# Performance work log

Measured on AMD Instinct MI355X. Metric: run time of the kernel, lower is better.

The kernel has to match this reference:

```python
import jax, jax.numpy as jnp
import numpy as np

N_QUBITS = 12
N_LAYERS = 5
OUTPUT_DIM = 4
BATCH = 1024


def _apply_1q(state, U, q, n):
    # state: (B, 2^n) complex; U: (B, 2, 2) per-sample unitary on wire q
    B = state.shape[0]
    s = state.reshape(B, 2 ** q, 2, -1)
    s = jnp.einsum('bik,bakc->baic', U, s)
    return s.reshape(B, -1)


def _cnot(state, c, t, n):
    # CNOT with control wire c, target wire t (wire 0 = most significant bit)
    B = state.shape[0]
    s = state.reshape((B,) + (2,) * n)
    s0 = jax.lax.index_in_dim(s, 0, axis=1 + c, keepdims=True)
    s1 = jax.lax.index_in_dim(s, 1, axis=1 + c, keepdims=True)
    s1 = jnp.flip(s1, axis=1 + t)  # X on target where control = 1
    return jnp.concatenate([s0, s1], axis=1 + c).reshape(B, -1)


def _forward(x, input_weights, theta, output_weights):
    n, L, D = N_QUBITS, N_LAYERS, OUTPUT_DIM
    x = jnp.tanh(x)
    B = x.shape[0]
    # |0...0> initial state, batched
    state = jnp.zeros((B, 2 ** n), jnp.complex64).at[:, 0].set(1.0)
    for l in range(L):
        # data re-uploading: RX(input_weights[l,j] * x[:,j]) on every wire, every layer
        a = input_weights[l][None, :] * x          # (B, n) RX angles
        b = theta[l, :, 0]                          # (n,) RY angles
        c = theta[l, :, 1]                          # (n,) RZ angles
        ca = jnp.cos(a / 2).astype(jnp.complex64)
        sa = jnp.sin(a / 2).astype(jnp.complex64)
        Rx = jnp.stack([jnp.stack([ca, -1j * sa], -1),
                        jnp.stack([-1j * sa, ca], -1)], -2)  # (B, n, 2, 2)
        cb = jnp.cos(b / 2).astype(jnp.complex64)
        sb = jnp.sin(b / 2).astype(jnp.complex64)
        ec = jnp.exp(-1j * c.astype(jnp.complex64) / 2)      # e^{-i c/2}
        # M = RZ(c) @ RY(b), shared across the batch
        M = jnp.stack([jnp.stack([ec * cb, -ec * sb], -1),
                       jnp.stack([jnp.conj(ec) * sb, jnp.conj(ec) * cb], -1)], -2)  # (n,2,2)
        # fused single-qubit unitary U = RZ @ RY @ RX per (sample, wire)
        U = jnp.einsum('qik,bqkj->bqij', M, Rx)
        for q in range(n):
            state = _apply_1q(state, U[:, q], q, n)
        for i in range(n):
            state = _cnot(state, i, (i + 1) % n, n)
    # exact <Z_i> on the first D wires
    p = jnp.abs(state) ** 2  # (B, 2^n)
    zs = []
    for i in range(D):
        pr = p.reshape(B, 2 ** i, 2, -1)
        zs.append(pr[:, :, 0, :].sum((1, 2)) - pr[:, :, 1, :].sum((1, 2)))
    Q = jnp.stack(zs, axis=1)  # (B, D)
    return output_weights[None, :] * Q


def setup_inputs() -> dict:
    key = jax.random.key(0)
    k1, k2, k3, k4 = jax.random.split(key, 4)
    return {
        'x': jax.random.normal(k1, (BATCH, N_QUBITS), jnp.float32),
        'input_weights': jax.random.normal(k2, (N_LAYERS, N_QUBITS), jnp.float32),
        'theta': jax.random.normal(k3, (N_LAYERS, N_QUBITS, 2), jnp.float32),
        'output_weights': jax.random.normal(k4, (OUTPUT_DIM,), jnp.float32),
    }


def reference(x, input_weights, theta, output_weights):
    return _forward(x, input_weights, theta, output_weights)
```

## Files before the change

kernel.cpp:

```cpp
#include <hip/hip_runtime.h>

#define NQ 12
#define NL 5
#define TPB 256


__device__ __forceinline__ void gate_pair(float2 &a, float2 &c,
        const float2 u00, const float2 u01, const float2 u10, const float2 u11) {
    float2 n0, n1;
    n0.x = fmaf(u00.x, a.x, fmaf(-u00.y, a.y, fmaf(u01.x, c.x, -u01.y * c.y)));
    n0.y = fmaf(u00.x, a.y, fmaf( u00.y, a.x, fmaf(u01.x, c.y,  u01.y * c.x)));
    n1.x = fmaf(u10.x, a.x, fmaf(-u10.y, a.y, fmaf(u11.x, c.x, -u11.y * c.y)));
    n1.y = fmaf(u10.x, a.y, fmaf( u10.y, a.x, fmaf(u11.x, c.y,  u11.y * c.x)));
    a = n0; c = n1;
}

template <int K>
__device__ __forceinline__ void apply_gate(float2 (&v)[16], const float2* __restrict__ Uq) {
    const float2 u00 = Uq[0], u01 = Uq[1], u10 = Uq[2], u11 = Uq[3];
#pragma unroll
    for (int h = 0; h < 8; ++h) {
        const int m0 = ((h >> K) << (K + 1)) | (h & ((1 << K) - 1));
        gate_pair(v[m0], v[m0 | (1 << K)], u00, u01, u10, u11);
    }
}

extern "C" __global__ void __launch_bounds__(TPB)
qnet_kernel(const float* __restrict__ x, const float* __restrict__ iw,
            const float* __restrict__ th, const float* __restrict__ ow,
            float* __restrict__ out) {
    __shared__ float2 st[4096];
    __shared__ float2 U[NL][NQ][4];
    __shared__ float wz[4][4];
    char* stb = (char*)st;

    const int b = blockIdx.x;
    const int tid = threadIdx.x;

    if (tid < NL * NQ) {
        const int l = tid / NQ, q = tid % NQ;
        const float xv = tanhf(x[b * NQ + q]);
        const float a = iw[l * NQ + q] * xv;
        const float bt = th[(l * NQ + q) * 2 + 0];
        const float ct = th[(l * NQ + q) * 2 + 1];
        float sa, ca; sincosf(0.5f * a, &sa, &ca);
        float sb, cb; sincosf(0.5f * bt, &sb, &cb);
        float sc, cc; sincosf(0.5f * ct, &sc, &cc);
        const float M00r = cc * cb, M00i = -sc * cb;
        const float M01r = -cc * sb, M01i = sc * sb;
        const float M10r = cc * sb, M10i = sc * sb;
        const float M11r = cc * cb, M11i = sc * cb;
        U[l][q][0] = make_float2(fmaf(M00r, ca,  sa * M01i), fmaf(M00i, ca, -sa * M01r));
        U[l][q][1] = make_float2(fmaf(ca, M01r,  sa * M00i), fmaf(ca, M01i, -sa * M00r));
        U[l][q][2] = make_float2(fmaf(M10r, ca,  sa * M11i), fmaf(M10i, ca, -sa * M11r));
        U[l][q][3] = make_float2(fmaf(ca, M11r,  sa * M10i), fmaf(ca, M11i, -sa * M10r));
    }

    const int baseA = (tid << 7) | ((tid & 7) << 4);
    const int baseB = ((tid >> 4) << 11) | ((tid & 15) << 3);
    const int baseC = (((tid >> 1) ^ ((tid >> 4) & 7)) << 4) | ((tid & 1) << 3);
    int pu = tid; pu ^= pu >> 1; pu ^= pu >> 2; pu ^= pu >> 4;
    const int Dt = pu ^ ((pu & 1) << 11);
    constexpr int CM[16] = {0x000,0x9FF,0xBFF,0x200,0xFFF,0x600,0x400,0xDFF,
                            0x7FF,0xE00,0xC00,0x5FF,0x800,0x1FF,0x3FF,0xA00};

    __syncthreads();

    float2 v[16];
    for (int l = 0; l < NL; ++l) {
        if (l == 0) {
#pragma unroll
            for (int r = 0; r < 16; ++r) v[r] = make_float2(0.f, 0.f);
            if (tid == 0) v[0].x = 1.f;
        } else {
#pragma unroll
            for (int c = 0; c < 8; ++c) {
                const float4 f = *(const float4*)(stb + (baseA ^ (c << 4)));
                v[2 * c]     = make_float2(f.x, f.y);
                v[2 * c + 1] = make_float2(f.z, f.w);
            }
        }
        apply_gate<0>(v, U[l][11]);
        apply_gate<1>(v, U[l][10]);
        apply_gate<2>(v, U[l][9]);
        apply_gate<3>(v, U[l][8]);
#pragma unroll
        for (int c = 0; c < 8; ++c) {
            *(float4*)(stb + (baseA ^ (c << 4))) =
                make_float4(v[2 * c].x, v[2 * c].y, v[2 * c + 1].x, v[2 * c + 1].y);
        }
        __syncthreads();

#pragma unroll
        for (int m = 0; m < 16; ++m)
            v[m] = *(const float2*)(stb + (baseB ^ ((m << 7) | ((m & 7) << 4))));
        apply_gate<0>(v, U[l][7]);
        apply_gate<1>(v, U[l][6]);
        apply_gate<2>(v, U[l][5]);
        apply_gate<3>(v, U[l][4]);
#pragma unroll
        for (int m = 0; m < 16; ++m)
            *(float2*)(stb + (baseB ^ ((m << 7) | ((m & 7) << 4)))) = v[m];
        __syncthreads();

#pragma unroll
        for (int m = 0; m < 16; ++m)
            v[m] = *(const float2*)(stb + baseC + (m << 11));
        apply_gate<0>(v, U[l][3]);
        apply_gate<1>(v, U[l][2]);
        apply_gate<2>(v, U[l][1]);
        apply_gate<3>(v, U[l][0]);
        __syncthreads();
#pragma unroll
        for (int m = 0; m < 16; ++m) {
            const int loc = Dt ^ CM[m];
            const int gl = loc >> 1;
            const int a = ((gl ^ ((gl >> 3) & 7)) << 4) | ((loc & 1) << 3);
            *(float2*)(stb + a) = v[m];
        }
        __syncthreads();
    }

    float ps = 0.f;
#pragma unroll
    for (int c = 0; c < 8; ++c) {
        const float4 f = *(const float4*)(stb + (baseA ^ (c << 4)));
        ps = fmaf(f.x, f.x, fmaf(f.y, f.y, fmaf(f.z, f.z, fmaf(f.w, f.w, ps))));
    }
    float s0 = (tid & 128) ? -ps : ps;
    float s1 = (tid & 64) ? -ps : ps;
    float s2 = (tid & 32) ? -ps : ps;
    float s3 = (tid & 16) ? -ps : ps;
#pragma unroll
    for (int off = 32; off > 0; off >>= 1) {
        s0 += __shfl_xor(s0, off);
        s1 += __shfl_xor(s1, off);
        s2 += __shfl_xor(s2, off);
        s3 += __shfl_xor(s3, off);
    }
    const int wave = tid >> 6;
    if ((tid & 63) == 0) {
        wz[wave][0] = s0; wz[wave][1] = s1; wz[wave][2] = s2; wz[wave][3] = s3;
    }
    __syncthreads();
    if (tid < 4) {
        const float z = wz[0][tid] + wz[1][tid] + wz[2][tid] + wz[3][tid];
        out[b * 4 + tid] = ow[tid] * z;
    }
}

extern "C" void kernel_launch(void* const* d_in, const int* in_sizes, int n_in,
                              void* d_out, int out_size, void* d_ws, size_t ws_size,
                              hipStream_t stream) {
    const float* x  = (const float*)d_in[0];
    const float* iw = (const float*)d_in[1];
    const float* th = (const float*)d_in[2];
    const float* ow = (const float*)d_in[3];
    float* out = (float*)d_out;
    const int batch = in_sizes[0] / NQ;
    hipLaunchKernelGGL(qnet_kernel, dim3(batch), dim3(TPB), 0, stream,
                       x, iw, th, ow, out);
}
```

Baseline: 47.35 us.

## Apply middle-qubit gates via DPP lane exchange to drop one LDS round-trip

Gates on wires 7,6 and 5,4 are now applied across lanes with DPP quad permutes, so each thread's amplitude set crosses lanes instead of going through shared memory. This removes one of the three shared-memory transpose phases and one barrier per layer. The swizzle and scatter addressing is rebuilt to match the new mapping. In exchange, each DPP gate does full-complex work on all 16 registers (twice the FMAs of a pair gate) and adds permute instructions.

```diff
diff --git a/kernel.cpp b/kernel.cpp
--- a/kernel.cpp
+++ b/kernel.cpp
@@ -4,6 +4,26 @@
 #define NL 5
 #define TPB 256
 
+__host__ __device__ constexpr int sfx12(int x) {
+    x ^= x >> 1; x ^= x >> 2; x ^= x >> 4; x ^= x >> 8;
+    return x & 0xFFF;
+}
+__host__ __device__ constexpr int amp_addr(int i) {
+    const int g = i >> 1;
+    const int G = g ^ ((g >> 3) & 7) ^ ((g >> 6) & 7);
+    return (G << 4) | ((i & 1) << 3);
+}
+__host__ __device__ constexpr int scat_c(int m) {
+    const int s = sfx12(m << 8);
+    return amp_addr(s ^ ((s & 1) << 11));
+}
+__host__ __device__ constexpr int p2_c(int m) { return amp_addr(m << 8); }
+
+template <int CTRL>
+__device__ __forceinline__ float dppx(float v) {
+    return __int_as_float(__builtin_amdgcn_update_dpp(
+        0, __float_as_int(v), CTRL, 0xF, 0xF, true));
+}
 
 __device__ __forceinline__ void gate_pair(float2 &a, float2 &c,
         const float2 u00, const float2 u01, const float2 u10, const float2 u11) {
@@ -25,17 +45,36 @@
     }
 }
 
+template <int CTRL, int LBIT>
+__device__ __forceinline__ void dpp_gate(float2 (&v)[16], const float2* __restrict__ Uq,
+                                         const int lane) {
+    const bool hi = (lane >> LBIT) & 1;
+    const float2 u00 = Uq[0], u01 = Uq[1], u10 = Uq[2], u11 = Uq[3];
+    const float2 co = hi ? u11 : u00;
+    const float2 cp = hi ? u10 : u01;
+#pragma unroll
+    for (int r = 0; r < 16; ++r) {
+        const float ox = v[r].x, oy = v[r].y;
+        const float px = dppx<CTRL>(ox);
+        const float py = dppx<CTRL>(oy);
+        v[r].x = fmaf(co.x, ox, fmaf(-co.y, oy, fmaf(cp.x, px, -cp.y * py)));
+        v[r].y = fmaf(co.x, oy, fmaf( co.y, ox, fmaf(cp.x, py,  cp.y * px)));
+    }
+}
+
 extern "C" __global__ void __launch_bounds__(TPB)
 qnet_kernel(const float* __restrict__ x, const float* __restrict__ iw,
             const float* __restrict__ th, const float* __restrict__ ow,
             float* __restrict__ out) {
     __shared__ float2 st[4096];
-    __shared__ float2 U[NL][NQ][4];
+    __shared__ __align__(16) float2 U[NL][NQ][4];
     __shared__ float wz[4][4];
     char* stb = (char*)st;
 
     const int b = blockIdx.x;
     const int tid = threadIdx.x;
+    const int Ln = tid & 63;
+    const int w  = tid >> 6;
 
     if (tid < NL * NQ) {
         const int l = tid / NQ, q = tid % NQ;
@@ -56,13 +95,11 @@
         U[l][q][3] = make_float2(fmaf(ca, M11r,  sa * M10i), fmaf(ca, M11i, -sa * M10r));
     }
 
-    const int baseA = (tid << 7) | ((tid & 7) << 4);
-    const int baseB = ((tid >> 4) << 11) | ((tid & 15) << 3);
-    const int baseC = (((tid >> 1) ^ ((tid >> 4) & 7)) << 4) | ((tid & 1) << 3);
-    int pu = tid; pu ^= pu >> 1; pu ^= pu >> 2; pu ^= pu >> 4;
-    const int Dt = pu ^ ((pu & 1) << 11);
-    constexpr int CM[16] = {0x000,0x9FF,0xBFF,0x200,0xFFF,0x600,0x400,0xDFF,
-                            0x7FF,0xE00,0xC00,0x5FF,0x800,0x1FF,0x3FF,0xA00};
+    const int base1 = amp_addr(tid << 4);
+    const int T2 = ((Ln & 3) << 6) | (w << 4) | (Ln >> 2);
+    const int base2 = amp_addr(T2);
+    const int sT = sfx12(T2);
+    const int baseS = amp_addr(sT ^ ((sT & 1) << 11));
 
     __syncthreads();
 
@@ -75,7 +112,7 @@
         } else {
 #pragma unroll
             for (int c = 0; c < 8; ++c) {
-                const float4 f = *(const float4*)(stb + (baseA ^ (c << 4)));
+                const float4 f = *(const float4*)(stb + (base1 ^ (c << 4)));
                 v[2 * c]     = make_float2(f.x, f.y);
                 v[2 * c + 1] = make_float2(f.z, f.w);
             }
@@ -84,47 +121,34 @@
         apply_gate<1>(v, U[l][10]);
         apply_gate<2>(v, U[l][9]);
         apply_gate<3>(v, U[l][8]);
+        dpp_gate<0xB1, 0>(v, U[l][7], Ln);
+        dpp_gate<0x4E, 1>(v, U[l][6], Ln);
 #pragma unroll
-        for (int c = 0; c < 8; ++c) {
-            *(float4*)(stb + (baseA ^ (c << 4))) =
+        for (int c = 0; c < 8; ++c)
+            *(float4*)(stb + (base1 ^ (c << 4))) =
                 make_float4(v[2 * c].x, v[2 * c].y, v[2 * c + 1].x, v[2 * c + 1].y);
-        }
         __syncthreads();
 
 #pragma unroll
         for (int m = 0; m < 16; ++m)
-            v[m] = *(const float2*)(stb + (baseB ^ ((m << 7) | ((m & 7) << 4))));
-        apply_gate<0>(v, U[l][7]);
-        apply_gate<1>(v, U[l][6]);
-        apply_gate<2>(v, U[l][5]);
-        apply_gate<3>(v, U[l][4]);
-#pragma unroll
-        for (int m = 0; m < 16; ++m)
-            *(float2*)(stb + (baseB ^ ((m << 7) | ((m & 7) << 4)))) = v[m];
-        __syncthreads();
-
-#pragma unroll
-        for (int m = 0; m < 16; ++m)
-            v[m] = *(const float2*)(stb + baseC + (m << 11));
+            v[m] = *(const float2*)(stb + (base2 ^ p2_c(m)));
+        dpp_gate<0xB1, 0>(v, U[l][5], Ln);
+        dpp_gate<0x4E, 1>(v, U[l][4], Ln);
         apply_gate<0>(v, U[l][3]);
         apply_gate<1>(v, U[l][2]);
         apply_gate<2>(v, U[l][1]);
         apply_gate<3>(v, U[l][0]);
         __syncthreads();
 #pragma unroll
-        for (int m = 0; m < 16; ++m) {
-            const int loc = Dt ^ CM[m];
-            const int gl = loc >> 1;
-            const int a = ((gl ^ ((gl >> 3) & 7)) << 4) | ((loc & 1) << 3);
-            *(float2*)(stb + a) = v[m];
-        }
+        for (int m = 0; m < 16; ++m)
+            *(float2*)(stb + (baseS ^ scat_c(m))) = v[m];
         __syncthreads();
     }
 
     float ps = 0.f;
 #pragma unroll
     for (int c = 0; c < 8; ++c) {
-        const float4 f = *(const float4*)(stb + (baseA ^ (c << 4)));
+        const float4 f = *(const float4*)(stb + (base1 ^ (c << 4)));
         ps = fmaf(f.x, f.x, fmaf(f.y, f.y, fmaf(f.z, f.z, fmaf(f.w, f.w, ps))));
     }
     float s0 = (tid & 128) ? -ps : ps;
@@ -138,9 +162,8 @@
         s2 += __shfl_xor(s2, off);
         s3 += __shfl_xor(s3, off);
     }
-    const int wave = tid >> 6;
     if ((tid & 63) == 0) {
-        wz[wave][0] = s0; wz[wave][1] = s1; wz[wave][2] = s2; wz[wave][3] = s3;
+        wz[w][0] = s0; wz[w][1] = s1; wz[w][2] = s2; wz[w][3] = s3;
     }
     __syncthreads();
     if (tid < 4) {
```

New measurement: 51.60 us. 9.0% more time.

## Exploit product-state first layer, drop intra-wave barrier, measure from registers

Applied to the files above, without the earlier changes.

Layer 0 acts on |0...0>, so the first two gate stages are computed as tensor products of the first columns of the single-qubit unitaries instead of full gate sweeps. The barrier between stage A and stage B is replaced by an LDS wait, relying on the data exchanged between those two stages staying inside a single wavefront. The final CNOT scatter is skipped and the Z expectations are computed directly from registers, using a precomputed parity mapping. Together these cut LDS traffic, barriers and arithmetic, at the cost of correctness depending on the intra-wave exchange assumption and on the constexpr index mappings.

```diff
diff --git a/kernel.cpp b/kernel.cpp
--- a/kernel.cpp
+++ b/kernel.cpp
@@ -4,7 +4,32 @@
 #define NL 5
 #define TPB 256
 
-
+__host__ __device__ constexpr int sfx12_(int x) {
+    x ^= x >> 1; x ^= x >> 2; x ^= x >> 4; x ^= x >> 8;
+    return x & 0xFFF;
+}
+__host__ __device__ constexpr int par_(int x) {
+    int y = x; y ^= y >> 8; y ^= y >> 4; y ^= y >> 2; y ^= y >> 1;
+    return y & 1;
+}
+__host__ __device__ constexpr int amp_addr(int i) {
+    const int g = i >> 1;
+    const int G = g ^ ((g >> 3) & 7);
+    return (G << 4) | ((i & 1) << 3);
+}
+__host__ __device__ constexpr int scat_c(int m) {
+    const int s = sfx12_(m << 8);
+    return amp_addr(s ^ ((s & 1) << 11));
+}
+__host__ __device__ constexpr int bpat(int m) { return amp_addr(m << 4); }
+__host__ __device__ constexpr int meas_h(int m) {
+    const int d = sfx12_(m << 8) ^ (par_(m) << 11);
+    return (d >> 8) & 15;
+}
+
+__device__ __forceinline__ float2 cmul(float2 a, float2 b) {
+    return make_float2(fmaf(a.x, b.x, -a.y * b.y), fmaf(a.x, b.y, a.y * b.x));
+}
 __device__ __forceinline__ void gate_pair(float2 &a, float2 &c,
         const float2 u00, const float2 u01, const float2 u10, const float2 u11) {
     float2 n0, n1;
@@ -14,7 +39,6 @@
     n1.y = fmaf(u10.x, a.y, fmaf( u10.y, a.x, fmaf(u11.x, c.y,  u11.y * c.x)));
     a = n0; c = n1;
 }
-
 template <int K>
 __device__ __forceinline__ void apply_gate(float2 (&v)[16], const float2* __restrict__ Uq) {
     const float2 u00 = Uq[0], u01 = Uq[1], u10 = Uq[2], u11 = Uq[3];
@@ -30,12 +54,13 @@
             const float* __restrict__ th, const float* __restrict__ ow,
             float* __restrict__ out) {
     __shared__ float2 st[4096];
-    __shared__ float2 U[NL][NQ][4];
+    __shared__ __align__(16) float2 U[NL][NQ][4];
     __shared__ float wz[4][4];
     char* stb = (char*)st;
 
     const int b = blockIdx.x;
     const int tid = threadIdx.x;
+    const int w = tid >> 6;
 
     if (tid < NL * NQ) {
         const int l = tid / NQ, q = tid % NQ;
@@ -56,22 +81,32 @@
         U[l][q][3] = make_float2(fmaf(ca, M11r,  sa * M10i), fmaf(ca, M11i, -sa * M10r));
     }
 
-    const int baseA = (tid << 7) | ((tid & 7) << 4);
-    const int baseB = ((tid >> 4) << 11) | ((tid & 15) << 3);
-    const int baseC = (((tid >> 1) ^ ((tid >> 4) & 7)) << 4) | ((tid & 1) << 3);
-    int pu = tid; pu ^= pu >> 1; pu ^= pu >> 2; pu ^= pu >> 4;
-    const int Dt = pu ^ ((pu & 1) << 11);
-    constexpr int CM[16] = {0x000,0x9FF,0xBFF,0x200,0xFFF,0x600,0x400,0xDFF,
-                            0x7FF,0xE00,0xC00,0x5FF,0x800,0x1FF,0x3FF,0xA00};
+    const int baseA = amp_addr(tid << 4);
+    const int baseB = amp_addr(((tid >> 4) << 8) | (tid & 15));
+    const int baseC = amp_addr(tid);
+    const int pt = __popc(tid) & 1;
+    const int baseS = amp_addr(sfx12_(tid) ^ (pt << 11));
+    const int hT = pt << 3;
 
     __syncthreads();
 
     float2 v[16];
     for (int l = 0; l < NL; ++l) {
         if (l == 0) {
-#pragma unroll
-            for (int r = 0; r < 16; ++r) v[r] = make_float2(0.f, 0.f);
-            if (tid == 0) v[0].x = 1.f;
+            float2 p[16];
+            p[0] = make_float2(1.f, 0.f);
+#pragma unroll
+            for (int k = 0; k < 4; ++k) {
+                const float2 u00 = U[0][11 - k][0], u10 = U[0][11 - k][2];
+#pragma unroll
+                for (int j = 0; j < (1 << k); ++j) {
+                    p[j | (1 << k)] = cmul(p[j], u10);
+                    p[j] = cmul(p[j], u00);
+                }
+            }
+            const float msk = (tid == 0) ? 1.f : 0.f;
+#pragma unroll
+            for (int r = 0; r < 16; ++r) v[r] = make_float2(p[r].x * msk, p[r].y * msk);
         } else {
 #pragma unroll
             for (int c = 0; c < 8; ++c) {
@@ -79,28 +114,46 @@
                 v[2 * c]     = make_float2(f.x, f.y);
                 v[2 * c + 1] = make_float2(f.z, f.w);
             }
+            apply_gate<0>(v, U[l][11]);
+            apply_gate<1>(v, U[l][10]);
+            apply_gate<2>(v, U[l][9]);
+            apply_gate<3>(v, U[l][8]);
         }
-        apply_gate<0>(v, U[l][11]);
-        apply_gate<1>(v, U[l][10]);
-        apply_gate<2>(v, U[l][9]);
-        apply_gate<3>(v, U[l][8]);
-#pragma unroll
-        for (int c = 0; c < 8; ++c) {
+#pragma unroll
+        for (int c = 0; c < 8; ++c)
             *(float4*)(stb + (baseA ^ (c << 4))) =
                 make_float4(v[2 * c].x, v[2 * c].y, v[2 * c + 1].x, v[2 * c + 1].y);
+        asm volatile("s_waitcnt lgkmcnt(0)" ::: "memory");
+
+        if (l == 0) {
+            float2 q[16];
+            q[0] = make_float2(1.f, 0.f);
+#pragma unroll
+            for (int k = 0; k < 4; ++k) {
+                const float2 u00 = U[0][7 - k][0], u10 = U[0][7 - k][2];
+#pragma unroll
+                for (int j = 0; j < (1 << k); ++j) {
+                    q[j | (1 << k)] = cmul(q[j], u10);
+                    q[j] = cmul(q[j], u00);
+                }
+            }
+            const float2 w0 = *(const float2*)(stb + ((tid & 15) << 3));
+            const float msk = (tid < 16) ? 1.f : 0.f;
+            const float2 ww = make_float2(w0.x * msk, w0.y * msk);
+#pragma unroll
+            for (int m = 0; m < 16; ++m) v[m] = cmul(q[m], ww);
+        } else {
+#pragma unroll
+            for (int m = 0; m < 16; ++m)
+                v[m] = *(const float2*)(stb + (baseB ^ bpat(m)));
+            apply_gate<0>(v, U[l][7]);
+            apply_gate<1>(v, U[l][6]);
+            apply_gate<2>(v, U[l][5]);
+            apply_gate<3>(v, U[l][4]);
         }
-        __syncthreads();
-
 #pragma unroll
         for (int m = 0; m < 16; ++m)
-            v[m] = *(const float2*)(stb + (baseB ^ ((m << 7) | ((m & 7) << 4))));
-        apply_gate<0>(v, U[l][7]);
-        apply_gate<1>(v, U[l][6]);
-        apply_gate<2>(v, U[l][5]);
-        apply_gate<3>(v, U[l][4]);
-#pragma unroll
-        for (int m = 0; m < 16; ++m)
-            *(float2*)(stb + (baseB ^ ((m << 7) | ((m & 7) << 4)))) = v[m];
+            *(float2*)(stb + (baseB ^ bpat(m))) = v[m];
         __syncthreads();
 
 #pragma unroll
@@ -110,37 +163,35 @@
         apply_gate<1>(v, U[l][2]);
         apply_gate<2>(v, U[l][1]);
         apply_gate<3>(v, U[l][0]);
-        __syncthreads();
-#pragma unroll
-        for (int m = 0; m < 16; ++m) {
-            const int loc = Dt ^ CM[m];
-            const int gl = loc >> 1;
-            const int a = ((gl ^ ((gl >> 3) & 7)) << 4) | ((loc & 1) << 3);
-            *(float2*)(stb + a) = v[m];
+
+        if (l < NL - 1) {
+            __syncthreads();
+#pragma unroll
+            for (int m = 0; m < 16; ++m)
+                *(float2*)(stb + (baseS ^ scat_c(m))) = v[m];
+            __syncthreads();
         }
-        __syncthreads();
-    }
-
-    float ps = 0.f;
-#pragma unroll
-    for (int c = 0; c < 8; ++c) {
-        const float4 f = *(const float4*)(stb + (baseA ^ (c << 4)));
-        ps = fmaf(f.x, f.x, fmaf(f.y, f.y, fmaf(f.z, f.z, fmaf(f.w, f.w, ps))));
-    }
-    float s0 = (tid & 128) ? -ps : ps;
-    float s1 = (tid & 64) ? -ps : ps;
-    float s2 = (tid & 32) ? -ps : ps;
-    float s3 = (tid & 16) ? -ps : ps;
+    }
+
+    float z0 = 0.f, z1 = 0.f, z2 = 0.f, z3 = 0.f;
+#pragma unroll
+    for (int m = 0; m < 16; ++m) {
+        const float pr = fmaf(v[m].x, v[m].x, v[m].y * v[m].y);
+        const int h = meas_h(m) ^ hT;
+        z0 += (h & 8) ? -pr : pr;
+        z1 += (h & 4) ? -pr : pr;
+        z2 += (h & 2) ? -pr : pr;
+        z3 += (h & 1) ? -pr : pr;
+    }
 #pragma unroll
     for (int off = 32; off > 0; off >>= 1) {
-        s0 += __shfl_xor(s0, off);
-        s1 += __shfl_xor(s1, off);
-        s2 += __shfl_xor(s2, off);
-        s3 += __shfl_xor(s3, off);
-    }
-    const int wave = tid >> 6;
+        z0 += __shfl_xor(z0, off);
+        z1 += __shfl_xor(z1, off);
+        z2 += __shfl_xor(z2, off);
+        z3 += __shfl_xor(z3, off);
+    }
     if ((tid & 63) == 0) {
-        wz[wave][0] = s0; wz[wave][1] = s1; wz[wave][2] = s2; wz[wave][3] = s3;
+        wz[w][0] = z0; wz[w][1] = z1; wz[w][2] = z2; wz[w][3] = z3;
     }
     __syncthreads();
     if (tid < 4) {
```

New measurement: 51.50 us. +8.8%, slower.
